# Kernel optimization log

Measured on AMD Instinct MI355X. Metric: run time of the kernel, lower is better.

The kernel has to match this reference:

```python
import jax, jax.numpy as jnp
import numpy as np

N = 20000   # nodes
IN = 128    # in_feats
H = 2       # n_heads
D = 32      # per-head dim (hid_feats = H*D = 64)
K = 3       # diffusion hops in AGDNConv
R = 5       # relations into dst type 'drug'
E = 320000  # edges per relation
NEG_SLOPE = 0.2


def setup_inputs() -> dict:
    key = jax.random.key(0)
    ks = jax.random.split(key, 11)
    s = 1.0 / np.sqrt(IN)
    return dict(
        h=jax.random.normal(ks[0], (N, IN), jnp.float32),
        src_idx=jax.random.randint(ks[1], (R, E), 0, N, dtype=jnp.int32),
        dst_idx=jax.random.randint(ks[2], (R, E), 0, N, dtype=jnp.int32),
        fc_w=jax.random.normal(ks[3], (R, IN, H * D), jnp.float32) * s,
        res_w=jax.random.normal(ks[4], (R, IN, H * D), jnp.float32) * s,
        attn_l=jax.random.normal(ks[5], (R, H, D), jnp.float32) * 0.1,
        attn_r=jax.random.normal(ks[6], (R, H, D), jnp.float32) * 0.1,
        hop_attn_l=jax.random.normal(ks[7], (R, H, D), jnp.float32) * 0.1,
        hop_attn_r=jax.random.normal(ks[8], (R, H, D), jnp.float32) * 0.1,
        w_rel=jax.random.normal(ks[9], (R, R), jnp.float32) * (1.0 / np.sqrt(R)),
        b_rel=jax.random.normal(ks[10], (R,), jnp.float32) * 0.1,
    )


def _agdn_conv(h, src, dst, fc_w, res_w, al, ar, hal, har):
    """One AGDNConv (GAT attention + K-hop diffusion + HA hop attention + residual)."""
    x = (h @ fc_w).reshape(N, H, D)                       # [N,H,D] projected feats
    el = jnp.sum(x * al, -1)                              # [N,H]
    er = jnp.sum(x * ar, -1)                              # [N,H]
    e = jax.nn.leaky_relu(el[src] + er[dst], NEG_SLOPE)   # [E,H] edge logits
    # segment softmax over incoming edges per dst node
    emax = jax.ops.segment_max(e, dst, num_segments=N)
    emax = jnp.where(jnp.isfinite(emax), emax, 0.0)
    ee = jnp.exp(e - emax[dst])
    denom = jax.ops.segment_sum(ee, dst, num_segments=N)
    alpha = ee / jnp.maximum(denom[dst], 1e-9)            # [E,H]

    def hop(hk, _):
        msg = alpha[:, :, None] * hk[src]                 # [E,H,D] gather+weight
        hk1 = jax.ops.segment_sum(msg, dst, num_segments=N)
        return hk1, hk1

    _, hks = jax.lax.scan(hop, x, None, length=K)         # [K,N,H,D]
    hops = jnp.concatenate([x[None], hks], axis=0)        # [K+1,N,H,D]
    # hop_norm: L2 normalize each hop's features
    hops = hops / jnp.maximum(jnp.linalg.norm(hops, axis=-1, keepdims=True), 1e-9)
    # HA hop attention
    hl = jnp.sum(hops * hal, -1)                          # [K+1,N,H]
    hr = jnp.sum(hops[0] * har, -1)                       # [N,H]
    hop_w = jax.nn.softmax(jax.nn.leaky_relu(hl + hr[None], NEG_SLOPE), axis=0)
    out = jnp.einsum('knh,knhd->nhd', hop_w, hops)        # [N,H,D]
    return out + (h @ res_w).reshape(N, H, D)             # residual


def reference(h, src_idx, dst_idx, fc_w, res_w, attn_l, attn_r, hop_attn_l, hop_attn_r, w_rel, b_rel):
    # per-relation AGDN convolutions (HeteroGraphConv dispatch)
    outs = jax.vmap(_agdn_conv, in_axes=(None, 0, 0, 0, 0, 0, 0, 0, 0))(
        h, src_idx, dst_idx, fc_w, res_w, attn_l, attn_r, hop_attn_l, hop_attn_r)  # [R,N,H,D]
    # my_agg_func2: learned relation weights = model_drug(ones(R))
    weights = w_rel @ jnp.ones((R,), jnp.float32) + b_rel  # [R]
    combined = jnp.einsum('r,rnhd->nhd', weights, outs)    # weighted relation sum
    return jnp.mean(combined, axis=1)                      # combine='mean' over heads -> [N,D]
```

## Files before the change

kernel.cpp:

```cpp
#include <hip/hip_runtime.h>
#include <hip/hip_bf16.h>

#define NN 20000
#define IN 128
#define HH 2
#define DD 32
#define HD 64
#define KK 3
#define RR 5
#define EE 320000
#define NEG 0.2f

#define PADK 136
#define NB 313
#define NBLK 64
#define CHUNK 5000
#define CAP 2048
#define NBCAP (NB * CAP)
#define RPS 20004

typedef short v8s __attribute__((ext_vector_type(8)));
typedef float v4f __attribute__((ext_vector_type(4)));
typedef _Float16 hf8 __attribute__((ext_vector_type(8)));

__device__ __forceinline__ ushort f2b(float f) {
    unsigned u = __float_as_uint(f);
    unsigned r = (u + 0x7fff + ((u >> 16) & 1)) >> 16;
    return (ushort)r;
}
__device__ __forceinline__ ushort f2h(float f) {
    _Float16 h = (_Float16)f;
    return __builtin_bit_cast(ushort, h);
}
__device__ __forceinline__ float h2f(ushort u) {
    _Float16 h = __builtin_bit_cast(_Float16, u);
    return (float)h;
}
__device__ __forceinline__ float2 up2(unsigned u) {
    return make_float2(h2f((ushort)(u & 0xFFFF)), h2f((ushort)(u >> 16)));
}

__global__ __launch_bounds__(256) void cvt_kernel(
    const float* __restrict__ fcw, const float* __restrict__ resw,
    ushort* __restrict__ wb, int* __restrict__ bcnt)
{
    int j = blockIdx.x * 256 + threadIdx.x;
    if (j < RR * NB) bcnt[j] = 0;
    if (j >= RR * 128 * IN) return;
    int k = j & 127;
    int c = (j >> 7) & 127;
    int r = j >> 14;
    float v = (c < HD) ? fcw[(r * IN + k) * HD + c] : resw[(r * IN + k) * HD + (c - HD)];
    wb[j] = f2b(v);
}

__global__ __launch_bounds__(256) void proj_mfma(
    const float* __restrict__ h, const ushort* __restrict__ wb,
    const float* __restrict__ attn_l, const float* __restrict__ attn_r,
    ushort* __restrict__ t0, ushort* __restrict__ resh,
    float* __restrict__ el, float* __restrict__ er)
{
    __shared__ ushort As[64 * PADK];
    __shared__ ushort Bs[128 * PADK];
    int bx = blockIdx.x;
    int r = bx / 313;
    int tile = bx - r * 313;
    int n0 = tile * 64;
    int tid = threadIdx.x;

    #pragma unroll
    for (int i = 0; i < 8; i++) {
        int c = tid + 256 * i;
        int row = c >> 5;
        int off = (c & 31) * 4;
        int gn = n0 + row;
        float4 v = make_float4(0.f, 0.f, 0.f, 0.f);
        if (gn < NN) v = *(const float4*)&h[(size_t)gn * IN + off];
        *(ushort4*)&As[row * PADK + off] =
            make_ushort4(f2b(v.x), f2b(v.y), f2b(v.z), f2b(v.w));
    }
    const ushort* wr = wb + (size_t)r * 128 * IN;
    #pragma unroll
    for (int i = 0; i < 8; i++) {
        int c = tid + 256 * i;
        int row = c >> 4;
        int off = (c & 15) * 8;
        *(uint4*)&Bs[row * PADK + off] = *(const uint4*)&wr[row * IN + off];
    }
    __syncthreads();

    int w = tid >> 6, lane = tid & 63;
    int lm = lane & 15, lq = lane >> 4;

    v4f acc[4][2];
    #pragma unroll
    for (int mt = 0; mt < 4; mt++)
        #pragma unroll
        for (int nt = 0; nt < 2; nt++) acc[mt][nt] = (v4f){0.f, 0.f, 0.f, 0.f};

    const ushort* Ab = &As[lm * PADK + lq * 8];
    const ushort* Bb = &Bs[(w * 32 + lm) * PADK + lq * 8];

    #pragma unroll
    for (int ks = 0; ks < 4; ks++) {
        v8s a[4], b[2];
        #pragma unroll
        for (int mt = 0; mt < 4; mt++) a[mt] = *(const v8s*)(Ab + mt * 16 * PADK + ks * 32);
        #pragma unroll
        for (int nt = 0; nt < 2; nt++) b[nt] = *(const v8s*)(Bb + nt * 16 * PADK + ks * 32);
        #pragma unroll
        for (int mt = 0; mt < 4; mt++)
            #pragma unroll
            for (int nt = 0; nt < 2; nt++)
                acc[mt][nt] = __builtin_amdgcn_mfma_f32_16x16x32_bf16(a[mt], b[nt], acc[mt][nt], 0, 0, 0);
    }

    int colbase = w * 32 + lm;
    #pragma unroll
    for (int mt = 0; mt < 4; mt++) {
        #pragma unroll
        for (int nt = 0; nt < 2; nt++) {
            int col = colbase + nt * 16;
            #pragma unroll
            for (int p = 0; p < 4; p++) {
                int node = n0 + mt * 16 + lq * 4 + p;
                if (node < NN) {
                    float v = acc[mt][nt][p];
                    if (col < HD) {
                        t0[((size_t)r * NN + node) * HD + col] = f2h(v);
                    } else {
                        resh[((size_t)r * NN + node) * HD + (col - HD)] = f2h(v);
                    }
                }
            }
        }
    }

    if (w < 2) {
        float al0 = attn_l[(r * HH + w) * DD + lm];
        float al1 = attn_l[(r * HH + w) * DD + lm + 16];
        float ar0 = attn_r[(r * HH + w) * DD + lm];
        float ar1 = attn_r[(r * HH + w) * DD + lm + 16];
        #pragma unroll
        for (int mt = 0; mt < 4; mt++) {
            #pragma unroll
            for (int p = 0; p < 4; p++) {
                float pl = acc[mt][0][p] * al0 + acc[mt][1][p] * al1;
                float pr = acc[mt][0][p] * ar0 + acc[mt][1][p] * ar1;
                #pragma unroll
                for (int off = 1; off < 16; off <<= 1) {
                    pl += __shfl_xor(pl, off, 64);
                    pr += __shfl_xor(pr, off, 64);
                }
                if (lm == 0) {
                    int node = n0 + mt * 16 + lq * 4 + p;
                    if (node < NN) {
                        el[((size_t)r * NN + node) * HH + w] = pl;
                        er[((size_t)r * NN + node) * HH + w] = pr;
                    }
                }
            }
        }
    }
}

__global__ __launch_bounds__(256) void part_kernel(
    const int* __restrict__ src, const int* __restrict__ dst,
    int* __restrict__ bcnt, unsigned* __restrict__ bucketRec)
{
    __shared__ int hh[NB];
    int r = blockIdx.x >> 6;
    int blk = blockIdx.x & 63;
    int tid = threadIdx.x;
    for (int i = tid; i < NB; i += 256) hh[i] = 0;
    __syncthreads();
    const int* S = src + (size_t)r * EE + blk * CHUNK;
    const int* D = dst + (size_t)r * EE + blk * CHUNK;
    for (int i = tid; i < CHUNK; i += 256)
        atomicAdd(&hh[D[i] >> 6], 1);
    __syncthreads();
    for (int i = tid; i < NB; i += 256) {
        int c = hh[i];
        hh[i] = c ? atomicAdd(&bcnt[r * NB + i], c) : 0;
    }
    __syncthreads();
    unsigned* BR = bucketRec + (size_t)r * NBCAP;
    for (int i = tid; i < CHUNK; i += 256) {
        int s = S[i], d = D[i];
        int b = d >> 6;
        int pos = atomicAdd(&hh[b], 1);
        if (pos < CAP)
            BR[((size_t)b << 11) + pos] = (unsigned)s | ((unsigned)(d & 63) << 15);
    }
}

__global__ __launch_bounds__(256) void bsort_alpha_kernel(
    const unsigned* __restrict__ bucketRec, const int* __restrict__ bcnt,
    const float* __restrict__ el, const float* __restrict__ er,
    uint2* __restrict__ csrE, int* __restrict__ rowp)
{
    __shared__ int cnt64s[64];
    __shared__ int segS[65];
    __shared__ int cur[64];
    __shared__ float2 erL[64];
    __shared__ float2 mx2[64];
    __shared__ float2 inv2[64];
    __shared__ unsigned sSD[CAP];
    __shared__ float2 sL[CAP];

    int bk = blockIdx.x;
    int r = bk / NB;
    int bkt = bk - r * NB;
    int tid = threadIdx.x;
    int cnt = bcnt[bk];
    if (cnt > CAP) cnt = CAP;

    if (tid < 64) {
        cnt64s[tid] = 0;
        int gn = bkt * 64 + tid;
        erL[tid] = (gn < NN) ? ((const float2*)er)[(size_t)r * NN + gn]
                             : make_float2(0.f, 0.f);
    }
    __syncthreads();
    const unsigned* BR = bucketRec + (size_t)bk * CAP;
    for (int i = tid; i < cnt; i += 256)
        atomicAdd(&cnt64s[(BR[i] >> 15) & 63], 1);
    __syncthreads();
    if (tid < 64) {
        int v = cnt64s[tid];
        int x = v;
        #pragma unroll
        for (int off = 1; off < 64; off <<= 1) {
            int tt = __shfl_up(x, off, 64);
            if (tid >= off) x += tt;
        }
        segS[tid] = x - v;
        cur[tid] = x - v;
        if (tid == 63) segS[64] = x;
    }
    __syncthreads();
    const float2* el2 = (const float2*)el + (size_t)r * NN;
    for (int i = tid; i < cnt; i += 256) {
        unsigned rec = BR[i];
        int s = rec & 0x7FFF;
        int d = (rec >> 15) & 63;
        float2 a = el2[s];
        float2 b = erL[d];
        float l0 = a.x + b.x; l0 = l0 > 0.f ? l0 : NEG * l0;
        float l1 = a.y + b.y; l1 = l1 > 0.f ? l1 : NEG * l1;
        int pos = atomicAdd(&cur[d], 1);
        sSD[pos] = rec;
        sL[pos] = make_float2(l0, l1);
    }
    __syncthreads();
    {
        int d = tid >> 2, sub = tid & 3;
        int b0 = segS[d], e0 = segS[d + 1];
        float m0 = -1e30f, m1 = -1e30f;
        for (int i = b0 + sub; i < e0; i += 4) {
            float2 l = sL[i];
            m0 = fmaxf(m0, l.x); m1 = fmaxf(m1, l.y);
        }
        m0 = fmaxf(m0, __shfl_xor(m0, 1, 64));
        m0 = fmaxf(m0, __shfl_xor(m0, 2, 64));
        m1 = fmaxf(m1, __shfl_xor(m1, 1, 64));
        m1 = fmaxf(m1, __shfl_xor(m1, 2, 64));
        float s0 = 0.f, s1 = 0.f;
        for (int i = b0 + sub; i < e0; i += 4) {
            float2 l = sL[i];
            s0 += __expf(l.x - m0); s1 += __expf(l.y - m1);
        }
        s0 += __shfl_xor(s0, 1, 64); s0 += __shfl_xor(s0, 2, 64);
        s1 += __shfl_xor(s1, 1, 64); s1 += __shfl_xor(s1, 2, 64);
        if (sub == 0) {
            mx2[d] = make_float2(m0, m1);
            inv2[d] = make_float2(1.f / fmaxf(s0, 1e-9f), 1.f / fmaxf(s1, 1e-9f));
            int gn = bkt * 64 + d;
            if (gn < NN) {
                int len = e0 - b0;
                rowp[r * RPS + gn] = (int)(((unsigned)(bkt * CAP + b0)) | ((unsigned)len << 20));
            }
        }
    }
    __syncthreads();
    uint2* E = csrE + (size_t)bk * CAP;
    for (int i = tid; i < cnt; i += 256) {
        unsigned rec = sSD[i];
        int d = (rec >> 15) & 63;
        float2 l = sL[i];
        float w0 = __expf(l.x - mx2[d].x) * inv2[d].x;
        float w1 = __expf(l.y - mx2[d].y) * inv2[d].y;
        E[i] = make_uint2(rec, (unsigned)f2h(w0) | ((unsigned)f2h(w1) << 16));
    }
}

__global__ __launch_bounds__(256) void hop_kernel(
    const ushort* __restrict__ tin, ushort* __restrict__ tout,
    const uint2* __restrict__ csrE, const int* __restrict__ rowp)
{
    int nb = gridDim.x;
    int q = nb >> 3, rmd = nb & 7;
    int xcd = blockIdx.x & 7, pos = blockIdx.x >> 3;
    int bid = (xcd < rmd ? xcd * (q + 1) : rmd * (q + 1) + (xcd - rmd) * q) + pos;

    int w = (bid * 256 + (int)threadIdx.x) >> 6;
    if (w >= RR * (NN / 8)) return;
    int lane = threadIdx.x & 63;
    int g = lane >> 3;
    int f = (lane & 7) * 8;
    int sh = ((lane >> 2) & 1) * 16;
    int r = w / (NN / 8);
    int n0 = (w - r * (NN / 8)) * 8;

    unsigned pv = (unsigned)rowp[r * RPS + n0 + g];
    int bg = (int)(pv & 0xFFFFF);
    int len = (int)(pv >> 20);
    int eg = bg + len;
    int cl = (len + 1) >> 1;
    int b2 = bg + cl;

    int m = cl;
    m = max(m, __shfl_xor(m, 8, 64));
    m = max(m, __shfl_xor(m, 16, 64));
    m = max(m, __shfl_xor(m, 32, 64));

    int lastA = bg + cl - 1;
    lastA = lastA > bg ? lastA : bg;
    int lastB = eg - 1;
    lastB = lastB > b2 ? lastB : b2;

    const ushort* T = tin + (size_t)r * NN * HD;
    const uint2* E = csrE + (size_t)r * NBCAP;

    float accA[8] = {0.f, 0.f, 0.f, 0.f, 0.f, 0.f, 0.f, 0.f};
    float accB[8] = {0.f, 0.f, 0.f, 0.f, 0.f, 0.f, 0.f, 0.f};
    #pragma unroll 4
    for (int j = 0; j < m; j++) {
        int ia = bg + j;
        int iac = ia < lastA ? ia : lastA;
        int ib = b2 + j;
        int ibc = ib < lastB ? ib : lastB;
        uint2 ra = E[iac];
        uint2 rb = E[ibc];
        float wa = (j < cl) ? h2f((ushort)(ra.y >> sh)) : 0.f;
        float wb = (ib < eg) ? h2f((ushort)(rb.y >> sh)) : 0.f;
        int na = (int)(ra.x & 0x7FFF); na = na < NN ? na : 0;
        int nbv = (int)(rb.x & 0x7FFF); nbv = nbv < NN ? nbv : 0;
        hf8 va = *(const hf8*)&T[(size_t)na * HD + f];
        hf8 vb = *(const hf8*)&T[(size_t)nbv * HD + f];
        #pragma unroll
        for (int k2 = 0; k2 < 8; k2++) {
            accA[k2] += wa * (float)va[k2];
            accB[k2] += wb * (float)vb[k2];
        }
    }
    ushort o[8];
    #pragma unroll
    for (int k = 0; k < 8; k++) o[k] = f2h(accA[k] + accB[k]);
    *(uint4*)&tout[((size_t)r * NN + n0 + g) * HD + f] = *(uint4*)o;
}

__global__ __launch_bounds__(256) void final_kernel(
    const ushort* __restrict__ t0, const ushort* __restrict__ t1,
    const ushort* __restrict__ t2, const ushort* __restrict__ t3,
    const ushort* __restrict__ resh,
    const float* __restrict__ hal, const float* __restrict__ har,
    const float* __restrict__ w_rel, const float* __restrict__ b_rel,
    float* __restrict__ out)
{
    int idx = blockIdx.x * 256 + threadIdx.x;
    if (idx >= NN * HH * 4) return;
    int fq = idx & 3;
    int h_ = (idx >> 2) & 1;
    int n = idx >> 3;
    const ushort* tb[4] = {t0, t1, t2, t3};
    float o[8];
    #pragma unroll
    for (int d = 0; d < 8; d++) o[d] = 0.f;

    for (int r = 0; r < RR; r++) {
        float wr = b_rel[r];
        #pragma unroll
        for (int j = 0; j < RR; j++) wr += w_rel[r * RR + j];
        const float* hp = hal + (r * HH + h_) * DD + fq * 8;
        const float* gp = har + (r * HH + h_) * DD + fq * 8;
        float4 ha0 = *(const float4*)hp;
        float4 ha1 = *(const float4*)(hp + 4);
        float4 hr0 = *(const float4*)gp;
        float4 hr1 = *(const float4*)(gp + 4);
        float halc[8] = {ha0.x, ha0.y, ha0.z, ha0.w, ha1.x, ha1.y, ha1.z, ha1.w};
        float harc[8] = {hr0.x, hr0.y, hr0.z, hr0.w, hr1.x, hr1.y, hr1.z, hr1.w};

        size_t tbase = ((size_t)r * NN + n) * HD + h_ * DD + fq * 8;
        uint4 tv[4];
        float sq[4], dl[4], dr = 0.f;
        #pragma unroll
        for (int k = 0; k < 4; k++) {
            tv[k] = *(const uint4*)(tb[k] + tbase);
            unsigned ww[4] = {tv[k].x, tv[k].y, tv[k].z, tv[k].w};
            float s = 0.f, d1 = 0.f;
            #pragma unroll
            for (int j = 0; j < 4; j++) {
                float2 v = up2(ww[j]);
                s  += v.x * v.x + v.y * v.y;
                d1 += v.x * halc[2 * j] + v.y * halc[2 * j + 1];
                if (k == 0)
                    dr += v.x * harc[2 * j] + v.y * harc[2 * j + 1];
            }
            sq[k] = s; dl[k] = d1;
        }
        #pragma unroll
        for (int k = 0; k < 4; k++) {
            sq[k] += __shfl_xor(sq[k], 1, 64); sq[k] += __shfl_xor(sq[k], 2, 64);
            dl[k] += __shfl_xor(dl[k], 1, 64); dl[k] += __shfl_xor(dl[k], 2, 64);
        }
        dr += __shfl_xor(dr, 1, 64); dr += __shfl_xor(dr, 2, 64);

        float inv[4], lg[4], mx = -1e30f;
        #pragma unroll
        for (int k = 0; k < 4; k++)
            inv[k] = 1.f / fmaxf(sqrtf(sq[k]), 1e-9f);
        #pragma unroll
        for (int k = 0; k < 4; k++) {
            float l = dl[k] * inv[k] + dr * inv[0];
            l = l > 0.f ? l : NEG * l;
            lg[k] = l;
            mx = fmaxf(mx, l);
        }
        float ssum = 0.f;
        #pragma unroll
        for (int k = 0; k < 4; k++) { lg[k] = __expf(lg[k] - mx); ssum += lg[k]; }
        float sw = wr / ssum;
        #pragma unroll
        for (int k = 0; k < 4; k++) {
            float coef = lg[k] * inv[k] * sw;
            unsigned ww[4] = {tv[k].x, tv[k].y, tv[k].z, tv[k].w};
            #pragma unroll
            for (int j = 0; j < 4; j++) {
                float2 v = up2(ww[j]);
                o[2 * j]     += coef * v.x;
                o[2 * j + 1] += coef * v.y;
            }
        }
        uint4 rv = *(const uint4*)(resh + tbase);
        unsigned rw[4] = {rv.x, rv.y, rv.z, rv.w};
        #pragma unroll
        for (int j = 0; j < 4; j++) {
            float2 v = up2(rw[j]);
            o[2 * j]     += wr * v.x;
            o[2 * j + 1] += wr * v.y;
        }
    }
    float p[8];
    #pragma unroll
    for (int j = 0; j < 8; j++) p[j] = __shfl_down(o[j], 4, 64);
    if (h_ == 0) {
        float4* op = (float4*)(out + (size_t)n * DD + fq * 8);
        op[0] = make_float4(0.5f * (o[0] + p[0]), 0.5f * (o[1] + p[1]),
                            0.5f * (o[2] + p[2]), 0.5f * (o[3] + p[3]));
        op[1] = make_float4(0.5f * (o[4] + p[4]), 0.5f * (o[5] + p[5]),
                            0.5f * (o[6] + p[6]), 0.5f * (o[7] + p[7]));
    }
}

extern "C" void kernel_launch(void* const* d_in, const int* in_sizes, int n_in,
                              void* d_out, int out_size, void* d_ws, size_t ws_size,
                              hipStream_t stream) {
    (void)in_sizes; (void)n_in; (void)out_size; (void)ws_size;
    const float* h     = (const float*)d_in[0];
    const int*   src   = (const int*)d_in[1];
    const int*   dst   = (const int*)d_in[2];
    const float* fcw   = (const float*)d_in[3];
    const float* resw  = (const float*)d_in[4];
    const float* atl   = (const float*)d_in[5];
    const float* atr   = (const float*)d_in[6];
    const float* hal   = (const float*)d_in[7];
    const float* har   = (const float*)d_in[8];
    const float* wrel  = (const float*)d_in[9];
    const float* brel  = (const float*)d_in[10];
    float* out = (float*)d_out;

    float* ws = (float*)d_ws;
    size_t off = 0;
    float* el   = ws + off;  off += (size_t)RR * NN * HH;
    float* er   = ws + off;  off += (size_t)RR * NN * HH;
    uint2* csrE = (uint2*)(ws + off);      off += (size_t)RR * NBCAP * 2;
    unsigned* bucketRec = (unsigned*)(ws + off); off += (size_t)RR * NBCAP;
    ushort* resh = (ushort*)(ws + off);    off += (size_t)RR * NN * HD / 2;
    ushort* t0  = (ushort*)(ws + off);     off += (size_t)RR * NN * HD / 2;
    ushort* t1  = (ushort*)(ws + off);     off += (size_t)RR * NN * HD / 2;
    ushort* t2  = (ushort*)(ws + off);     off += (size_t)RR * NN * HD / 2;
    ushort* t3  = (ushort*)(ws + off);     off += (size_t)RR * NN * HD / 2;
    ushort* wb  = (ushort*)(ws + off);     off += (size_t)RR * 128 * IN / 2;
    int* rowp   = (int*)(ws + off);  off += (size_t)RR * RPS;
    int* bcnt   = (int*)(ws + off);  off += (size_t)RR * NB;

    cvt_kernel<<<(RR * 128 * IN + 255) / 256, 256, 0, stream>>>(fcw, resw, wb, bcnt);
    proj_mfma<<<313 * RR, 256, 0, stream>>>(h, wb, atl, atr, t0, resh, el, er);
    part_kernel<<<RR * NBLK, 256, 0, stream>>>(src, dst, bcnt, bucketRec);
    bsort_alpha_kernel<<<RR * NB, 256, 0, stream>>>(bucketRec, bcnt, el, er, csrE, rowp);
    hop_kernel<<<(RR * (NN / 8) + 3) / 4, 256, 0, stream>>>(t0, t1, csrE, rowp);
    hop_kernel<<<(RR * (NN / 8) + 3) / 4, 256, 0, stream>>>(t1, t2, csrE, rowp);
    hop_kernel<<<(RR * (NN / 8) + 3) / 4, 256, 0, stream>>>(t2, t3, csrE, rowp);
    final_kernel<<<(NN * HH * 4 + 255) / 256, 256, 0, stream>>>(t0, t1, t2, t3, resh, hal, har, wrel, brel, out);
}
```

Baseline: 249.5 us.

## Pre-convert h to bf16, privatize bucket histograms, software-pipeline hop gathers

The input h is now converted to bf16 once in cvt_kernel, so proj_mfma loads bf16 rows directly instead of re-reading and converting fp32 h for each of the five relations. The per-bucket histogram in bsort_alpha is split into per-wave copies to cut LDS atomic contention, and the copies are summed before the scan. The hop kernel prefetches edge records two steps ahead and feature rows one step ahead, so gather latency overlaps with the accumulation. The cost is an extra bf16 copy of h in the workspace, more registers in the hop loop, and a larger cvt launch.

New measurement: 236.4 us. -5.2%, faster.

```diff
diff --git a/kernel.cpp b/kernel.cpp
--- a/kernel.cpp
+++ b/kernel.cpp
@@ -18,6 +18,7 @@
 #define CAP 2048
 #define NBCAP (NB * CAP)
 #define RPS 20004
+#define HTOT (NN * IN / 4)
 
 typedef short v8s __attribute__((ext_vector_type(8)));
 typedef float v4f __attribute__((ext_vector_type(4)));
@@ -41,21 +42,28 @@
 }
 
 __global__ __launch_bounds__(256) void cvt_kernel(
-    const float* __restrict__ fcw, const float* __restrict__ resw,
-    ushort* __restrict__ wb, int* __restrict__ bcnt)
+    const float* __restrict__ h, const float* __restrict__ fcw,
+    const float* __restrict__ resw, ushort* __restrict__ wb,
+    ushort* __restrict__ hb, int* __restrict__ bcnt)
 {
     int j = blockIdx.x * 256 + threadIdx.x;
     if (j < RR * NB) bcnt[j] = 0;
-    if (j >= RR * 128 * IN) return;
-    int k = j & 127;
-    int c = (j >> 7) & 127;
-    int r = j >> 14;
-    float v = (c < HD) ? fcw[(r * IN + k) * HD + c] : resw[(r * IN + k) * HD + (c - HD)];
-    wb[j] = f2b(v);
+    if (j < RR * 128 * IN) {
+        int k = j & 127;
+        int c = (j >> 7) & 127;
+        int r = j >> 14;
+        float v = (c < HD) ? fcw[(r * IN + k) * HD + c] : resw[(r * IN + k) * HD + (c - HD)];
+        wb[j] = f2b(v);
+    }
+    int t = j - RR * 128 * IN;
+    if (t >= 0 && t < HTOT) {
+        float4 v = ((const float4*)h)[t];
+        ((ushort4*)hb)[t] = make_ushort4(f2b(v.x), f2b(v.y), f2b(v.z), f2b(v.w));
+    }
 }
 
 __global__ __launch_bounds__(256) void proj_mfma(
-    const float* __restrict__ h, const ushort* __restrict__ wb,
+    const ushort* __restrict__ hb, const ushort* __restrict__ wb,
     const float* __restrict__ attn_l, const float* __restrict__ attn_r,
     ushort* __restrict__ t0, ushort* __restrict__ resh,
     float* __restrict__ el, float* __restrict__ er)
@@ -69,15 +77,14 @@
     int tid = threadIdx.x;
 
     #pragma unroll
-    for (int i = 0; i < 8; i++) {
+    for (int i = 0; i < 4; i++) {
         int c = tid + 256 * i;
-        int row = c >> 5;
-        int off = (c & 31) * 4;
+        int row = c >> 4;
+        int off = (c & 15) * 8;
         int gn = n0 + row;
-        float4 v = make_float4(0.f, 0.f, 0.f, 0.f);
-        if (gn < NN) v = *(const float4*)&h[(size_t)gn * IN + off];
-        *(ushort4*)&As[row * PADK + off] =
-            make_ushort4(f2b(v.x), f2b(v.y), f2b(v.z), f2b(v.w));
+        uint4 v = make_uint4(0u, 0u, 0u, 0u);
+        if (gn < NN) v = *(const uint4*)&hb[(size_t)gn * IN + off];
+        *(uint4*)&As[row * PADK + off] = v;
     }
     const ushort* wr = wb + (size_t)r * 128 * IN;
     #pragma unroll
@@ -199,7 +206,7 @@
     const float* __restrict__ el, const float* __restrict__ er,
     uint2* __restrict__ csrE, int* __restrict__ rowp)
 {
-    __shared__ int cnt64s[64];
+    __shared__ int cnt64s[4][64];
     __shared__ int segS[65];
     __shared__ int cur[64];
     __shared__ float2 erL[64];
@@ -212,11 +219,13 @@
     int r = bk / NB;
     int bkt = bk - r * NB;
     int tid = threadIdx.x;
+    int wv = tid >> 6;
     int cnt = bcnt[bk];
     if (cnt > CAP) cnt = CAP;
 
     if (tid < 64) {
-        cnt64s[tid] = 0;
+        cnt64s[0][tid] = 0; cnt64s[1][tid] = 0;
+        cnt64s[2][tid] = 0; cnt64s[3][tid] = 0;
         int gn = bkt * 64 + tid;
         erL[tid] = (gn < NN) ? ((const float2*)er)[(size_t)r * NN + gn]
                              : make_float2(0.f, 0.f);
@@ -224,10 +233,10 @@
     __syncthreads();
     const unsigned* BR = bucketRec + (size_t)bk * CAP;
     for (int i = tid; i < cnt; i += 256)
-        atomicAdd(&cnt64s[(BR[i] >> 15) & 63], 1);
+        atomicAdd(&cnt64s[wv][(BR[i] >> 15) & 63], 1);
     __syncthreads();
     if (tid < 64) {
-        int v = cnt64s[tid];
+        int v = cnt64s[0][tid] + cnt64s[1][tid] + cnt64s[2][tid] + cnt64s[3][tid];
         int x = v;
         #pragma unroll
         for (int off = 1; off < 64; off <<= 1) {
@@ -298,8 +307,8 @@
     const ushort* __restrict__ tin, ushort* __restrict__ tout,
     const uint2* __restrict__ csrE, const int* __restrict__ rowp)
 {
-    int nb = gridDim.x;
-    int q = nb >> 3, rmd = nb & 7;
+    int nbk = gridDim.x;
+    int q = nbk >> 3, rmd = nbk & 7;
     int xcd = blockIdx.x & 7, pos = blockIdx.x >> 3;
     int bid = (xcd < rmd ? xcd * (q + 1) : rmd * (q + 1) + (xcd - rmd) * q) + pos;
 
@@ -332,27 +341,39 @@
     const ushort* T = tin + (size_t)r * NN * HD;
     const uint2* E = csrE + (size_t)r * NBCAP;
 
+    int iA0 = bg < lastA ? bg : lastA;
+    int iA1 = bg + 1 < lastA ? bg + 1 : lastA;
+    int iB0 = b2 < lastB ? b2 : lastB;
+    int iB1 = b2 + 1 < lastB ? b2 + 1 : lastB;
+    uint2 raC = E[iA0], rbC = E[iB0];
+    uint2 raN = E[iA1], rbN = E[iB1];
+    int na0 = (int)(raC.x & 0x7FFF); na0 = na0 < NN ? na0 : 0;
+    int nb0 = (int)(rbC.x & 0x7FFF); nb0 = nb0 < NN ? nb0 : 0;
+    hf8 fa = *(const hf8*)&T[(size_t)na0 * HD + f];
+    hf8 fb = *(const hf8*)&T[(size_t)nb0 * HD + f];
+
     float accA[8] = {0.f, 0.f, 0.f, 0.f, 0.f, 0.f, 0.f, 0.f};
     float accB[8] = {0.f, 0.f, 0.f, 0.f, 0.f, 0.f, 0.f, 0.f};
-    #pragma unroll 4
+    #pragma unroll 2
     for (int j = 0; j < m; j++) {
-        int ia = bg + j;
-        int iac = ia < lastA ? ia : lastA;
-        int ib = b2 + j;
-        int ibc = ib < lastB ? ib : lastB;
-        uint2 ra = E[iac];
-        uint2 rb = E[ibc];
-        float wa = (j < cl) ? h2f((ushort)(ra.y >> sh)) : 0.f;
-        float wb = (ib < eg) ? h2f((ushort)(rb.y >> sh)) : 0.f;
-        int na = (int)(ra.x & 0x7FFF); na = na < NN ? na : 0;
-        int nbv = (int)(rb.x & 0x7FFF); nbv = nbv < NN ? nbv : 0;
-        hf8 va = *(const hf8*)&T[(size_t)na * HD + f];
-        hf8 vb = *(const hf8*)&T[(size_t)nbv * HD + f];
+        int ja = bg + j + 2; ja = ja < lastA ? ja : lastA;
+        int jb = b2 + j + 2; jb = jb < lastB ? jb : lastB;
+        uint2 ra2 = E[ja];
+        uint2 rb2 = E[jb];
+        int na1 = (int)(raN.x & 0x7FFF); na1 = na1 < NN ? na1 : 0;
+        int nb1 = (int)(rbN.x & 0x7FFF); nb1 = nb1 < NN ? nb1 : 0;
+        hf8 fa1 = *(const hf8*)&T[(size_t)na1 * HD + f];
+        hf8 fb1 = *(const hf8*)&T[(size_t)nb1 * HD + f];
+        float wa = (j < cl) ? h2f((ushort)(raC.y >> sh)) : 0.f;
+        float wb = (b2 + j < eg) ? h2f((ushort)(rbC.y >> sh)) : 0.f;
         #pragma unroll
         for (int k2 = 0; k2 < 8; k2++) {
-            accA[k2] += wa * (float)va[k2];
-            accB[k2] += wb * (float)vb[k2];
-        }
+            accA[k2] += wa * (float)fa[k2];
+            accB[k2] += wb * (float)fb[k2];
+        }
+        raC = raN; raN = ra2;
+        rbC = rbN; rbN = rb2;
+        fa = fa1; fb = fb1;
     }
     ushort o[8];
     #pragma unroll
@@ -492,11 +513,12 @@
     ushort* t2  = (ushort*)(ws + off);     off += (size_t)RR * NN * HD / 2;
     ushort* t3  = (ushort*)(ws + off);     off += (size_t)RR * NN * HD / 2;
     ushort* wb  = (ushort*)(ws + off);     off += (size_t)RR * 128 * IN / 2;
+    ushort* hb  = (ushort*)(ws + off);     off += (size_t)NN * IN / 2;
     int* rowp   = (int*)(ws + off);  off += (size_t)RR * RPS;
     int* bcnt   = (int*)(ws + off);  off += (size_t)RR * NB;
 
-    cvt_kernel<<<(RR * 128 * IN + 255) / 256, 256, 0, stream>>>(fcw, resw, wb, bcnt);
-    proj_mfma<<<313 * RR, 256, 0, stream>>>(h, wb, atl, atr, t0, resh, el, er);
+    cvt_kernel<<<(RR * 128 * IN + HTOT + 255) / 256, 256, 0, stream>>>(h, fcw, resw, wb, hb, bcnt);
+    proj_mfma<<<313 * RR, 256, 0, stream>>>(hb, wb, atl, atr, t0, resh, el, er);
     part_kernel<<<RR * NBLK, 256, 0, stream>>>(src, dst, bcnt, bucketRec);
     bsort_alpha_kernel<<<RR * NB, 256, 0, stream>>>(bucketRec, bcnt, el, er, csrE, rowp);
     hop_kernel<<<(RR * (NN / 8) + 3) / 4, 256, 0, stream>>>(t0, t1, csrE, rowp);
```
